# Kernel optimization log

Hardware: AMD Instinct MI355X
Metric: run time of the kernel (lower is better)

## Reference

```python
import jax, jax.numpy as jnp
import numpy as np

B, T, C = 256, 256, 384
HEADS = 6
HEAD_DIM = C // HEADS
WINDOW = 64


def setup_inputs() -> dict:
    key = jax.random.key(0)
    ks = jax.random.split(key, 5)
    scale = 0.02
    return {
        "x": jax.random.normal(ks[0], (B, T, C), dtype=jnp.float32),
        "qkv_w": jax.random.normal(ks[1], (C, 3 * C), dtype=jnp.float32) * scale,
        "qkv_b": jax.random.normal(ks[2], (3 * C,), dtype=jnp.float32) * scale,
        "proj_w": jax.random.normal(ks[3], (C, C), dtype=jnp.float32) * scale,
        "proj_b": jax.random.normal(ks[4], (C,), dtype=jnp.float32) * scale,
        "gate": jnp.ones((C,), dtype=jnp.float32),
    }


def reference(x, qkv_w, qkv_b, proj_w, proj_b, gate):
    Bx, Tx, Cx = x.shape
    qkv = x @ qkv_w + qkv_b                     # [B, T, 3C]
    q, k, v = jnp.split(qkv, 3, axis=-1)
    # [B, T, H, hd] -> [B, H, T, hd]
    q = q.reshape(Bx, Tx, HEADS, HEAD_DIM).transpose(0, 2, 1, 3)
    k = k.reshape(Bx, Tx, HEADS, HEAD_DIM).transpose(0, 2, 1, 3)
    v = v.reshape(Bx, Tx, HEADS, HEAD_DIM).transpose(0, 2, 1, 3)

    att = jnp.einsum("bhqd,bhkd->bhqk", q, k) * (1.0 / np.sqrt(HEAD_DIM).astype(np.float32))
    idx = jnp.arange(Tx)
    causal = idx[:, None] >= idx[None, :]                 # j <= i
    local = jnp.abs(idx[:, None] - idx[None, :]) <= WINDOW
    mask = (causal & local)[None, None, :, :]             # [1,1,T,T]
    att = jnp.where(mask, att, -jnp.inf)
    att = jax.nn.softmax(att, axis=-1)

    out = jnp.einsum("bhqk,bhkd->bhqd", att, v)           # [B, H, T, hd]
    out = out.transpose(0, 2, 1, 3).reshape(Bx, Tx, Cx)
    return (out * gate) @ proj_w + proj_b
```

## Files before the change

kernel.cpp:

```cpp
#include <hip/hip_runtime.h>
#include <hip/hip_bf16.h>

typedef unsigned short u16;
typedef __attribute__((ext_vector_type(8))) short short8;
typedef __attribute__((ext_vector_type(8))) unsigned short ushort8;
typedef __attribute__((ext_vector_type(4))) float f32x4;
typedef __attribute__((ext_vector_type(4))) float f4;

#define GLB_CAST(p) ((const __attribute__((address_space(1))) unsigned int*)(p))
#define LDS_CAST(p) ((__attribute__((address_space(3))) unsigned int*)(p))

__device__ __forceinline__ void gl_lds16(const void* g, void* l) {
  __builtin_amdgcn_global_load_lds(GLB_CAST(g), LDS_CAST(l), 16, 0, 0);
}

__device__ __forceinline__ u16 f2bf(float f) {
  __hip_bfloat16 b = __float2bfloat16(f);
  return __builtin_bit_cast(u16, b);
}
__device__ __forceinline__ float bf2f(u16 u) {
  unsigned int x = ((unsigned int)u) << 16;
  return __builtin_bit_cast(float, x);
}

__global__ void transpose_cvt_k(const float* __restrict__ in,
                                u16* __restrict__ out, int R, int C) {
  __shared__ float tile[32][33];
  int c0 = blockIdx.x * 32, r0 = blockIdx.y * 32;
  int tx = threadIdx.x, ty = threadIdx.y;
#pragma unroll
  for (int i = 0; i < 32; i += 8)
    tile[ty + i][tx] = in[(size_t)(r0 + ty + i) * C + c0 + tx];
  __syncthreads();
#pragma unroll
  for (int i = 0; i < 32; i += 8)
    out[(size_t)(c0 + ty + i) * R + r0 + tx] = f2bf(tile[tx][ty + i]);
}

template <int EPI>
__global__ __launch_bounds__(256, 2) void gemm_k(
    const void* __restrict__ Av, const u16* __restrict__ Bt,
    const float* __restrict__ bias,
    u16* __restrict__ oQ, u16* __restrict__ oK, u16* __restrict__ oVT,
    float* __restrict__ oF) {
  constexpr int K = 384;
  constexpr int NT = (EPI == 1) ? 9 : 3;
  __shared__ u16 As[64 * 384];
  __shared__ u16 Bs[4][3][1024];
  __shared__ u16 Rs[4][512];
  __shared__ u16 bias_sh[NT * 128];

  const int tid = threadIdx.x;
  const int m0 = blockIdx.x * 64;
  const int lane = tid & 63, wid = tid >> 6;
  const int lo = lane & 15, hi = lane >> 4;
  const int wc = wid;

  for (int i = tid; i < NT * 128; i += 256) bias_sh[i] = f2bf(bias[i]);

  const int bcol = wc * 32 + (lane >> 2);
  const int bc = ((lane & 3) ^ ((lane >> 3) & 3)) * 8;
  char* const slot_l = (char*)&Bs[0][0][0] + wid * 6144 + lane * 16;
  auto stageB = [&](int slot, int tn, int kt) {
    const u16* s = Bt + (size_t)(tn * 128 + bcol) * K + kt * 32 + bc;
    char* d = slot_l + slot * 2048;
    gl_lds16(s, d);
    gl_lds16(s + 16 * K, d + 1024);
  };

  stageB(0, 0, 0);
  stageB(1, 0, 1);

  if (EPI == 1) {
    const float* X = (const float*)Av;
#pragma unroll
    for (int i = 0; i < 12; ++i) {
      int c = tid + i * 256;
      int row = c / 48, cc = c % 48;
      const float* src = X + (size_t)(m0 + row) * K + cc * 8;
      f4 a = __builtin_nontemporal_load((const f4*)src);
      f4 b = __builtin_nontemporal_load((const f4*)(src + 4));
      ushort8 o;
#pragma unroll
      for (int j = 0; j < 4; ++j) { o[j] = f2bf(a[j]); o[4 + j] = f2bf(b[j]); }
      *(ushort8*)((char*)As + row * 768 + ((cc * 16) ^ ((row & 7) << 4))) = o;
    }
  } else {
    const u16* Ab = (const u16*)Av;
#pragma unroll
    for (int i = 0; i < 12; ++i) {
      int c = tid + i * 256;
      int row = c / 48, cc = c % 48;
      ushort8 v = __builtin_nontemporal_load(
          (const ushort8*)(Ab + (size_t)(m0 + row) * K + cc * 8));
      *(ushort8*)((char*)As + row * 768 + ((cc * 16) ^ ((row & 7) << 4))) = v;
    }
  }
  __syncthreads();

  const int akey = (lo & 7) << 4;
  const int rk = ((lo >> 1) & 3) << 4;
  int abase[4];
#pragma unroll
  for (int m = 0; m < 4; ++m) abase[m] = (m * 16 + lo) * 768;
  const int bbase = lo * 64 + (hi * 16 ^ rk);
  const char* const Asc = (const char*)As;
  const char* const sb0 = (const char*)&Bs[0][0][0] + wid * 6144;
  char* const rp_ = (char*)&Rs[0][0] + wid * 1024;

  const f32x4 Z4 = {0.f, 0.f, 0.f, 0.f};

  for (int t = 0; t < NT; ++t) {
    f32x4 acc[4][2];
#pragma unroll
    for (int m = 0; m < 4; ++m) { acc[m][0] = Z4; acc[m][1] = Z4; }

#pragma unroll
    for (int kt = 0; kt < 12; ++kt) {
      if (kt == 0) asm volatile("s_waitcnt vmcnt(4)" ::: "memory");
      else         asm volatile("s_waitcnt vmcnt(2)" ::: "memory");

      const char* sb = sb0 + (kt % 3) * 2048;
      short8 af[4], bf[2];
#pragma unroll
      for (int m = 0; m < 4; ++m)
        af[m] = *(const short8*)(Asc + abase[m] + ((kt * 64 + hi * 16) ^ akey));
      bf[0] = *(const short8*)(sb + bbase);
      bf[1] = *(const short8*)(sb + 1024 + bbase);

      if (kt < 10)           stageB((kt + 2) % 3, t, kt + 2);
      else if (t + 1 < NT)   stageB((kt + 2) % 3, t + 1, kt - 10);

      __builtin_amdgcn_s_setprio(1);
#pragma unroll
      for (int m = 0; m < 4; ++m) {
        acc[m][0] = __builtin_amdgcn_mfma_f32_16x16x32_bf16(af[m], bf[0], acc[m][0], 0, 0, 0);
        acc[m][1] = __builtin_amdgcn_mfma_f32_16x16x32_bf16(af[m], bf[1], acc[m][1], 0, 0, 0);
      }
      __builtin_amdgcn_s_setprio(0);
    }

    float bs0 = bf2f(bias_sh[t * 128 + wc * 32 + lo]);
    float bs1 = bf2f(bias_sh[t * 128 + wc * 32 + 16 + lo]);

    if (EPI == 1) {
      const int r3 = t / 3;
      u16* dst = (r3 == 0) ? oQ : ((r3 == 1) ? oK : oVT);
      const int hcb = (t - r3 * 3) * 128 + wc * 32;
      if (r3 < 2) {
#pragma unroll
        for (int p = 0; p < 4; ++p) {
#pragma unroll
          for (int n = 0; n < 2; ++n)
#pragma unroll
            for (int rr = 0; rr < 4; ++rr)
              *(u16*)(rp_ + (hi * 4 + rr) * 64 + (n * 16 + lo) * 2) =
                  f2bf(acc[p][n][rr] + (n ? bs1 : bs0));
          ushort8 v = *(const ushort8*)(rp_ + (lane >> 2) * 64 + (lane & 3) * 16);
          int hc = hcb + (lane & 3) * 8;
          int gm = m0 + p * 16 + (lane >> 2);
          *(ushort8*)(dst + (((size_t)((gm >> 8) * 6 + (hc >> 6))) << 14) +
                      (gm & 255) * 64 + (hc & 63)) = v;
        }
      } else {
#pragma unroll
        for (int p = 0; p < 4; ++p) {
#pragma unroll
          for (int n = 0; n < 2; ++n)
#pragma unroll
            for (int rr = 0; rr < 4; ++rr)
              *(u16*)(rp_ + (n * 16 + lo) * 32 + (hi * 4 + rr) * 2) =
                  f2bf(acc[p][n][rr] + (n ? bs1 : bs0));
          ushort8 v = *(const ushort8*)(rp_ + (lane >> 1) * 32 + (lane & 1) * 16);
          int hc = hcb + (lane >> 1);
          int tg = (m0 & 255) + p * 16 + (lane & 1) * 8;
          *(ushort8*)(dst + (((size_t)((m0 >> 8) * 6 + (hc >> 6))) << 14) +
                      (hc & 63) * 256 + tg) = v;
        }
      }
    } else {
      const int colb = t * 128 + wc * 32 + lo;
#pragma unroll
      for (int m = 0; m < 4; ++m)
#pragma unroll
        for (int rr = 0; rr < 4; ++rr) {
          int gm = m0 + m * 16 + hi * 4 + rr;
          __builtin_nontemporal_store(acc[m][0][rr] + bs0, &oF[(size_t)gm * 384 + colb]);
          __builtin_nontemporal_store(acc[m][1][rr] + bs1, &oF[(size_t)gm * 384 + colb + 16]);
        }
    }
  }
}

__global__ __launch_bounds__(256) void attn_k(
    const u16* __restrict__ Qb, const u16* __restrict__ Kb,
    const u16* __restrict__ VTb, const float* __restrict__ gate,
    u16* __restrict__ Ao) {
  __shared__ u16 Ks[128 * 64];
  __shared__ u16 Vs[64 * 128];
  __shared__ u16 Ps[4][16 * 128];
  const int bx = blockIdx.x;
  const int qt = bx & 3, bh = bx >> 2;
  const int h = bh % 6, b = bh / 6;
  const int i0 = qt * 64, j0 = i0 - 64;
  const int tid = threadIdx.x, w = tid >> 6, lane = tid & 63;
  const int lo = lane & 15, hi = lane >> 4;

  const u16* Kh = Kb + (size_t)bh * (256 * 64);
  const u16* Vh = VTb + (size_t)bh * (64 * 256);
  const u16* Qh = Qb + (size_t)bh * (256 * 64);

#pragma unroll
  for (int it = 0; it < 4; ++it) {
    int chunk = tid + it * 256;
    int row = chunk >> 3, cc = chunk & 7;
    int csrc = cc ^ (row & 7);
    int j = j0 + row; if (j < 0) j = 0;
    gl_lds16(Kh + j * 64 + csrc * 8, Ks + chunk * 8);
  }
#pragma unroll
  for (int it = 0; it < 4; ++it) {
    int chunk = tid + it * 256;
    int d = chunk >> 4, kc = chunk & 15;
    int ksrc = kc ^ (d & 7);
    int j = j0 + ksrc * 8; if (j < 0) j = 0;
    gl_lds16(Vh + d * 256 + j, Vs + chunk * 8);
  }

  const int iq = i0 + w * 16 + lo;
  short8 aq0 = *(const short8*)(Qh + iq * 64 + hi * 8);
  short8 aq1 = *(const short8*)(Qh + iq * 64 + 32 + hi * 8);

  __syncthreads();

  const f32x4 Z4 = {0.f, 0.f, 0.f, 0.f};
  f32x4 accS[8];
#pragma unroll
  for (int t = 0; t < 8; ++t) accS[t] = Z4;
#pragma unroll
  for (int t = 0; t < 8; ++t) {
    int key = t * 16 + lo;
    int base = key * 128;
    int sw = (key & 7) << 4;
    short8 bk0 = *(const short8*)((const char*)Ks + ((base + hi * 16) ^ sw));
    short8 bk1 = *(const short8*)((const char*)Ks + ((base + 64 + hi * 16) ^ sw));
    accS[t] = __builtin_amdgcn_mfma_f32_16x16x32_bf16(aq0, bk0, accS[t], 0, 0, 0);
    accS[t] = __builtin_amdgcn_mfma_f32_16x16x32_bf16(aq1, bk1, accS[t], 0, 0, 0);
  }

  float pv[4][8];
  float rinv[4];
#pragma unroll
  for (int r = 0; r < 4; ++r) {
    int i = i0 + w * 16 + hi * 4 + r;
    float mx = -1e30f;
    float vals[8];
#pragma unroll
    for (int t = 0; t < 8; ++t) {
      int j = j0 + t * 16 + lo;
      float s = accS[t][r] * 0.125f;
      bool ok = (j >= 0) && (j <= i) && (j >= i - 64);
      vals[t] = ok ? s : -1e30f;
      mx = fmaxf(mx, vals[t]);
    }
#pragma unroll
    for (int off = 1; off < 16; off <<= 1) mx = fmaxf(mx, __shfl_xor(mx, off));
    float sum = 0.f;
#pragma unroll
    for (int t = 0; t < 8; ++t) {
      float p = __expf(vals[t] - mx);
      pv[r][t] = p;
      sum += p;
    }
#pragma unroll
    for (int off = 1; off < 16; off <<= 1) sum += __shfl_xor(sum, off);
    rinv[r] = 1.0f / sum;
  }

  u16* Pw = Ps[w];
#pragma unroll
  for (int r = 0; r < 4; ++r) {
    int ql = hi * 4 + r;
    int sw = (ql & 7) << 4;
#pragma unroll
    for (int t = 0; t < 8; ++t) {
      int off = (ql * 256 + (t * 16 + lo) * 2) ^ sw;
      *(u16*)((char*)Pw + off) = f2bf(pv[r][t]);
    }
  }

  f32x4 accO[4];
#pragma unroll
  for (int dt = 0; dt < 4; ++dt) accO[dt] = Z4;
#pragma unroll
  for (int ks = 0; ks < 4; ++ks) {
    int offA = (lo * 256 + ks * 64 + hi * 16) ^ ((lo & 7) << 4);
    short8 ap = *(const short8*)((const char*)Pw + offA);
#pragma unroll
    for (int dt = 0; dt < 4; ++dt) {
      int d = dt * 16 + lo;
      int offB = (d * 256 + ks * 64 + hi * 16) ^ ((d & 7) << 4);
      short8 bv = *(const short8*)((const char*)Vs + offB);
      accO[dt] = __builtin_amdgcn_mfma_f32_16x16x32_bf16(ap, bv, accO[dt], 0, 0, 0);
    }
  }

#pragma unroll
  for (int dt = 0; dt < 4; ++dt) {
    int d = dt * 16 + lo;
    float gg = gate[h * 64 + d];
#pragma unroll
    for (int r = 0; r < 4; ++r) {
      int i = i0 + w * 16 + hi * 4 + r;
      float v = accO[dt][r] * rinv[r] * gg;
      Ao[(size_t)(b * 256 + i) * 384 + h * 64 + d] = f2bf(v);
    }
  }
}

extern "C" void kernel_launch(void* const* d_in, const int* in_sizes, int n_in,
                              void* d_out, int out_size, void* d_ws, size_t ws_size,
                              hipStream_t stream) {
  const float* x      = (const float*)d_in[0];
  const float* qkv_w  = (const float*)d_in[1];
  const float* qkv_b  = (const float*)d_in[2];
  const float* proj_w = (const float*)d_in[3];
  const float* proj_b = (const float*)d_in[4];
  const float* gate   = (const float*)d_in[5];
  float* out = (float*)d_out;

  char* ws = (char*)d_ws;
  u16* att  = (u16*)ws;
  u16* vT   = (u16*)(ws + 50331648);
  u16* w1T  = (u16*)(ws + 100663296);
  u16* pT   = (u16*)(ws + 101548032);
  u16* qbuf = (u16*)d_out;
  u16* kbuf = (u16*)((char*)d_out + 50331648);

  transpose_cvt_k<<<dim3(36, 12), dim3(32, 8), 0, stream>>>(qkv_w, w1T, 384, 1152);
  transpose_cvt_k<<<dim3(12, 12), dim3(32, 8), 0, stream>>>(proj_w, pT, 384, 384);

  gemm_k<1><<<1024, 256, 0, stream>>>(x, w1T, qkv_b, qbuf, kbuf, vT, nullptr);
  attn_k<<<256 * 6 * 4, 256, 0, stream>>>(qbuf, kbuf, vT, gate, att);
  gemm_k<2><<<1024, 256, 0, stream>>>(att, pT, proj_b, nullptr, nullptr, nullptr, out);
}
```

Baseline: 188.2 us.

## Halve GEMM row tile to 32 and write QKV epilogue directly without LDS staging

Both GEMM kernels now use 32-row M tiles instead of 64, doubling the grid to 2048 blocks and raising launch bounds to 3 blocks per SM. LDS usage drops and the per-wave accumulator count halves. The QKV epilogue no longer repacks through an LDS buffer into 16-byte vector stores and instead writes scattered 2-byte stores straight to global memory. This trades fewer, wider stores for more occupancy, but it also reloads the weight matrix twice as many times.

```diff
diff --git a/kernel.cpp b/kernel.cpp
--- a/kernel.cpp
+++ b/kernel.cpp
@@ -38,20 +38,19 @@
 }
 
 template <int EPI>
-__global__ __launch_bounds__(256, 2) void gemm_k(
+__global__ __launch_bounds__(256, 3) void gemm_k(
     const void* __restrict__ Av, const u16* __restrict__ Bt,
     const float* __restrict__ bias,
     u16* __restrict__ oQ, u16* __restrict__ oK, u16* __restrict__ oVT,
     float* __restrict__ oF) {
   constexpr int K = 384;
   constexpr int NT = (EPI == 1) ? 9 : 3;
-  __shared__ u16 As[64 * 384];
+  __shared__ u16 As[32 * 384];
   __shared__ u16 Bs[4][3][1024];
-  __shared__ u16 Rs[4][512];
   __shared__ u16 bias_sh[NT * 128];
 
   const int tid = threadIdx.x;
-  const int m0 = blockIdx.x * 64;
+  const int m0 = blockIdx.x * 32;
   const int lane = tid & 63, wid = tid >> 6;
   const int lo = lane & 15, hi = lane >> 4;
   const int wc = wid;
@@ -74,7 +73,7 @@
   if (EPI == 1) {
     const float* X = (const float*)Av;
 #pragma unroll
-    for (int i = 0; i < 12; ++i) {
+    for (int i = 0; i < 6; ++i) {
       int c = tid + i * 256;
       int row = c / 48, cc = c % 48;
       const float* src = X + (size_t)(m0 + row) * K + cc * 8;
@@ -88,7 +87,7 @@
   } else {
     const u16* Ab = (const u16*)Av;
 #pragma unroll
-    for (int i = 0; i < 12; ++i) {
+    for (int i = 0; i < 6; ++i) {
       int c = tid + i * 256;
       int row = c / 48, cc = c % 48;
       ushort8 v = __builtin_nontemporal_load(
@@ -100,20 +99,30 @@
 
   const int akey = (lo & 7) << 4;
   const int rk = ((lo >> 1) & 3) << 4;
-  int abase[4];
-#pragma unroll
-  for (int m = 0; m < 4; ++m) abase[m] = (m * 16 + lo) * 768;
+  int abase[2];
+#pragma unroll
+  for (int m = 0; m < 2; ++m) abase[m] = (m * 16 + lo) * 768;
   const int bbase = lo * 64 + (hi * 16 ^ rk);
   const char* const Asc = (const char*)As;
   const char* const sb0 = (const char*)&Bs[0][0][0] + wid * 6144;
-  char* const rp_ = (char*)&Rs[0][0] + wid * 1024;
+
+  int rqk[2][4], rv[2][4];
+#pragma unroll
+  for (int m = 0; m < 2; ++m)
+#pragma unroll
+    for (int rr = 0; rr < 4; ++rr) {
+      int gm = m0 + m * 16 + hi * 4 + rr;
+      int b = gm >> 8, tt = gm & 255;
+      rqk[m][rr] = b * 98304 + tt * 64;
+      rv[m][rr] = b * 98304 + tt;
+    }
 
   const f32x4 Z4 = {0.f, 0.f, 0.f, 0.f};
 
   for (int t = 0; t < NT; ++t) {
-    f32x4 acc[4][2];
-#pragma unroll
-    for (int m = 0; m < 4; ++m) { acc[m][0] = Z4; acc[m][1] = Z4; }
+    f32x4 acc[2][2];
+#pragma unroll
+    for (int m = 0; m < 2; ++m) { acc[m][0] = Z4; acc[m][1] = Z4; }
 
 #pragma unroll
     for (int kt = 0; kt < 12; ++kt) {
@@ -121,9 +130,9 @@
       else         asm volatile("s_waitcnt vmcnt(2)" ::: "memory");
 
       const char* sb = sb0 + (kt % 3) * 2048;
-      short8 af[4], bf[2];
-#pragma unroll
-      for (int m = 0; m < 4; ++m)
+      short8 af[2], bf[2];
+#pragma unroll
+      for (int m = 0; m < 2; ++m)
         af[m] = *(const short8*)(Asc + abase[m] + ((kt * 64 + hi * 16) ^ akey));
       bf[0] = *(const short8*)(sb + bbase);
       bf[1] = *(const short8*)(sb + 1024 + bbase);
@@ -133,7 +142,7 @@
 
       __builtin_amdgcn_s_setprio(1);
 #pragma unroll
-      for (int m = 0; m < 4; ++m) {
+      for (int m = 0; m < 2; ++m) {
         acc[m][0] = __builtin_amdgcn_mfma_f32_16x16x32_bf16(af[m], bf[0], acc[m][0], 0, 0, 0);
         acc[m][1] = __builtin_amdgcn_mfma_f32_16x16x32_bf16(af[m], bf[1], acc[m][1], 0, 0, 0);
       }
@@ -146,42 +155,24 @@
     if (EPI == 1) {
       const int r3 = t / 3;
       u16* dst = (r3 == 0) ? oQ : ((r3 == 1) ? oK : oVT);
-      const int hcb = (t - r3 * 3) * 128 + wc * 32;
-      if (r3 < 2) {
-#pragma unroll
-        for (int p = 0; p < 4; ++p) {
-#pragma unroll
-          for (int n = 0; n < 2; ++n)
-#pragma unroll
-            for (int rr = 0; rr < 4; ++rr)
-              *(u16*)(rp_ + (hi * 4 + rr) * 64 + (n * 16 + lo) * 2) =
-                  f2bf(acc[p][n][rr] + (n ? bs1 : bs0));
-          ushort8 v = *(const ushort8*)(rp_ + (lane >> 2) * 64 + (lane & 3) * 16);
-          int hc = hcb + (lane & 3) * 8;
-          int gm = m0 + p * 16 + (lane >> 2);
-          *(ushort8*)(dst + (((size_t)((gm >> 8) * 6 + (hc >> 6))) << 14) +
-                      (gm & 255) * 64 + (hc & 63)) = v;
-        }
-      } else {
-#pragma unroll
-        for (int p = 0; p < 4; ++p) {
-#pragma unroll
-          for (int n = 0; n < 2; ++n)
-#pragma unroll
-            for (int rr = 0; rr < 4; ++rr)
-              *(u16*)(rp_ + (n * 16 + lo) * 32 + (hi * 4 + rr) * 2) =
-                  f2bf(acc[p][n][rr] + (n ? bs1 : bs0));
-          ushort8 v = *(const ushort8*)(rp_ + (lane >> 1) * 32 + (lane & 1) * 16);
-          int hc = hcb + (lane >> 1);
-          int tg = (m0 & 255) + p * 16 + (lane & 1) * 8;
-          *(ushort8*)(dst + (((size_t)((m0 >> 8) * 6 + (hc >> 6))) << 14) +
-                      (hc & 63) * 256 + tg) = v;
-        }
+      const int hcb = (t - r3 * 3) * 128 + wc * 32 + lo;
+#pragma unroll
+      for (int n = 0; n < 2; ++n) {
+        int hc = hcb + n * 16;
+        float bs = n ? bs1 : bs0;
+        int cp = (r3 < 2) ? (((hc >> 6) << 14) + (hc & 63))
+                          : (((hc >> 6) << 14) + (hc & 63) * 256);
+        const int (*rp)[4] = (r3 < 2) ? rqk : rv;
+#pragma unroll
+        for (int m = 0; m < 2; ++m)
+#pragma unroll
+          for (int rr = 0; rr < 4; ++rr)
+            dst[(size_t)(rp[m][rr] + cp)] = f2bf(acc[m][n][rr] + bs);
       }
     } else {
       const int colb = t * 128 + wc * 32 + lo;
 #pragma unroll
-      for (int m = 0; m < 4; ++m)
+      for (int m = 0; m < 2; ++m)
 #pragma unroll
         for (int rr = 0; rr < 4; ++rr) {
           int gm = m0 + m * 16 + hi * 4 + rr;
@@ -340,7 +331,7 @@
   transpose_cvt_k<<<dim3(36, 12), dim3(32, 8), 0, stream>>>(qkv_w, w1T, 384, 1152);
   transpose_cvt_k<<<dim3(12, 12), dim3(32, 8), 0, stream>>>(proj_w, pT, 384, 384);
 
-  gemm_k<1><<<1024, 256, 0, stream>>>(x, w1T, qkv_b, qbuf, kbuf, vT, nullptr);
+  gemm_k<1><<<2048, 256, 0, stream>>>(x, w1T, qkv_b, qbuf, kbuf, vT, nullptr);
   attn_k<<<256 * 6 * 4, 256, 0, stream>>>(qbuf, kbuf, vT, gate, att);
-  gemm_k<2><<<1024, 256, 0, stream>>>(att, pT, proj_b, nullptr, nullptr, nullptr, out);
-}
+  gemm_k<2><<<2048, 256, 0, stream>>>(att, pT, proj_b, nullptr, nullptr, nullptr, out);
+}
```

Measured after the change: 283.1 us. 50.5% more time.
